# Kernel optimization log

Hardware: AMD Instinct MI355X
Metric: run time of the kernel (lower is better)

## Reference

```python
import jax, jax.numpy as jnp
import numpy as np

C = 256
CK = C // 8  # key/query channels


def setup_inputs() -> dict:
    key = jax.random.key(0)
    ks = jax.random.split(key, 7)
    B, H, W = 8, 64, 64
    x = jax.random.normal(ks[0], (B, C, H, W), dtype=jnp.float32)
    # 1x1 conv weights (out_ch, in_ch) and biases. Spectral norm is a weight
    # reparameterization; at forward time it is just a conv with (normalized)
    # weights, so we sample weights directly.
    Wf = jax.random.normal(ks[1], (CK, C), dtype=jnp.float32) * 0.02
    bf = jnp.zeros((CK,), dtype=jnp.float32)
    Wg = jax.random.normal(ks[2], (CK, C), dtype=jnp.float32) * 0.02
    bg = jnp.zeros((CK,), dtype=jnp.float32)
    Wh = jax.random.normal(ks[3], (C, C), dtype=jnp.float32) * 0.02
    bh = jnp.zeros((C,), dtype=jnp.float32)
    gamma = jnp.ones((1,), dtype=jnp.float32) * 0.5  # nonzero so attention path matters
    return {"x": x, "Wf": Wf, "bf": bf, "Wg": Wg, "bg": bg, "Wh": Wh, "bh": bh, "gamma": gamma}


def reference(x, Wf, bf, Wg, bg, Wh, bh, gamma):
    b, c, h, w = x.shape
    n = h * w
    xf = x.reshape(b, c, n)  # [B, C, N]
    # 1x1 convs == per-pixel linear maps
    fx = jnp.einsum("kc,bcn->bkn", Wf, xf) + bf[None, :, None]  # [B, CK, N]
    gx = jnp.einsum("kc,bcn->bkn", Wg, xf) + bg[None, :, None]  # [B, CK, N]
    hx = jnp.einsum("oc,bcn->bon", Wh, xf) + bh[None, :, None]  # [B, C, N]
    # sx[b, i, j] = <fx[:, i], gx[:, j]>
    sx = jnp.einsum("bki,bkj->bij", fx, gx)  # [B, N, N]
    # torch F.softmax(sx, dim=1): normalize over the first N axis (i)
    beta = jax.nn.softmax(sx, axis=1)
    ox = jnp.einsum("bci,bij->bcj", hx, beta).reshape(b, c, h, w)
    return gamma.reshape(()) * ox + x
```

## Files before the change

### kernel.cpp

```cpp
#include <hip/hip_runtime.h>
#include <stdint.h>


typedef __bf16 bf16;
typedef __bf16 bf16x2 __attribute__((ext_vector_type(2)));
typedef __bf16 bf16x8 __attribute__((ext_vector_type(8)));
typedef float  f32x16 __attribute__((ext_vector_type(16)));
typedef float  f32x4  __attribute__((ext_vector_type(4)));
typedef unsigned char u8;
typedef long   i64;

#define BATCH 8
#define CC    256
#define CKK   32
#define NN    4096
#define LOG2E 1.4426950408889634f

__device__ __forceinline__ f32x16 zero16() {
  f32x16 z;
#pragma unroll
  for (int i = 0; i < 16; ++i) z[i] = 0.0f;
  return z;
}

__device__ __forceinline__ unsigned pack2(float lo, float hi) {
  bf16x2 v = {(bf16)lo, (bf16)hi};
  return __builtin_bit_cast(unsigned, v);
}

__device__ __forceinline__ f32x16 mfma32(bf16x8 a, bf16x8 b, f32x16 c) {
  return __builtin_amdgcn_mfma_f32_32x32x16_bf16(a, b, c, 0, 0, 0);
}

__device__ __forceinline__ f32x16 mfma8(i64 a, i64 b, f32x16 c) {
  return __builtin_amdgcn_mfma_f32_32x32x16_fp8_fp8(a, b, c, 0, 0, 0);
}

#define GLDS16(srcp, dstp)                                                         \
  __builtin_amdgcn_global_load_lds(                                               \
      (const __attribute__((address_space(1))) void*)(srcp),                      \
      (__attribute__((address_space(3))) void*)(dstp), 16, 0, 0)

__global__ __launch_bounds__(256) void k_transpose(const float* __restrict__ x,
                                                   bf16* __restrict__ xT) {
  __shared__ float tile[64][65];
  const int n0 = blockIdx.x * 64;
  const int c0 = blockIdx.y * 64;
  const int b  = blockIdx.z;
  const int t = threadIdx.x;
  const int tn = t & 63, trow = t >> 6;
#pragma unroll
  for (int i = 0; i < 16; ++i) {
    int c = trow + i * 4;
    tile[c][tn] = x[((size_t)(b * CC + c0 + c)) * NN + n0 + tn];
  }
  __syncthreads();
#pragma unroll
  for (int i = 0; i < 16; ++i) {
    int n = trow + i * 4;
    xT[((size_t)(b * NN + n0 + n)) * CC + c0 + tn] = (bf16)tile[tn][n];
  }
}

__global__ __launch_bounds__(64) void k_wprep(const float* __restrict__ Wf, const float* __restrict__ bfv,
                                              const float* __restrict__ Wg, const float* __restrict__ bg,
                                              const float* __restrict__ Wh, const float* __restrict__ bh,
                                              bf16* __restrict__ Wcat, float* __restrict__ bcat) {
  const int ko = blockIdx.x;
  const int t = threadIdx.x;
  const float* src;
  float scale = 1.0f;
  if (ko < 32) src = Wf + (size_t)ko * CC;
  else if (ko < 64) { src = Wg + (size_t)(ko - 32) * CC; scale = LOG2E; }
  else src = Wh + (size_t)(ko - 64) * CC;
#pragma unroll
  for (int i = 0; i < 4; ++i)
    Wcat[(size_t)ko * CC + t + i * 64] = (bf16)(src[t + i * 64] * scale);
  if (ko == 0) {
    for (int i = t; i < 320; i += 64) {
      float v = (i < 32) ? bfv[i] : (i < 64) ? bg[i - 32] * LOG2E : bh[i - 64];
      bcat[i] = v;
    }
  }
}

__global__ __launch_bounds__(256, 2) void k_proj(const bf16* __restrict__ xT,
                                                 const bf16* __restrict__ Wcat,
                                                 const float* __restrict__ bcat,
                                                 bf16* __restrict__ fxT, bf16* __restrict__ gxT,
                                                 u8* __restrict__ hx8) {
  const int d = blockIdx.x;
  const int half = d >> 8;
  const int r = d & 255;
  const int b = r & 7, nb = r >> 3;
  const int t = threadIdx.x;
  const int w = t >> 6, ln = t & 63, ln31 = ln & 31, h = ln >> 5;
  const int n = nb * 128 + w * 32 + ln31;

  f32x16 acc[5];
#pragma unroll
  for (int m = 0; m < 5; ++m) acc[m] = zero16();

  const bf16* xrow = xT + ((size_t)(b * NN + n)) * CC;
#pragma unroll
  for (int ks = 0; ks < 16; ++ks) {
    bf16x8 bfrag = *(const bf16x8*)(xrow + ks * 16 + h * 8);
#pragma unroll
    for (int m = 0; m < 5; ++m) {
      const int mt = half * 5 + m;
      bf16x8 afrag = *(const bf16x8*)(Wcat + (size_t)(mt * 32 + ln31) * CC + ks * 16 + h * 8);
      acc[m] = mfma32(afrag, bfrag, acc[m]);
    }
  }

#pragma unroll
  for (int m = 0; m < 5; ++m) {
    const int mt = half * 5 + m;
#pragma unroll
    for (int q = 0; q < 4; ++q) {
      const int ko0 = mt * 32 + 8 * q + 4 * h;
      float v0 = acc[m][4 * q + 0] + bcat[ko0 + 0];
      float v1 = acc[m][4 * q + 1] + bcat[ko0 + 1];
      float v2 = acc[m][4 * q + 2] + bcat[ko0 + 2];
      float v3 = acc[m][4 * q + 3] + bcat[ko0 + 3];
      if (mt < 2) {
        bf16* dst = (mt == 0 ? fxT : gxT) + ((size_t)(b * NN + n)) * CKK + (8 * q + 4 * h);
        uint2 pv;
        pv.x = pack2(v0, v1);
        pv.y = pack2(v2, v3);
        *(uint2*)dst = pv;
      } else {
        const int c = ko0 - 64;
        unsigned wpk = (unsigned)__builtin_amdgcn_cvt_pk_fp8_f32(v0, v1, 0, false);
        wpk = (unsigned)__builtin_amdgcn_cvt_pk_fp8_f32(v2, v3, (int)wpk, true);
        u8* hp = hx8 + ((size_t)(b * CC + c)) * NN + n;
        hp[0]      = (u8)(wpk & 0xff);
        hp[NN]     = (u8)((wpk >> 8) & 0xff);
        hp[2 * NN] = (u8)((wpk >> 16) & 0xff);
        hp[3 * NN] = (u8)(wpk >> 24);
      }
    }
  }
}

__global__ __launch_bounds__(512, 2) void k_attn(const bf16* __restrict__ fxT,
                                                 const bf16* __restrict__ gxT,
                                                 const u8* __restrict__ hx8,
                                                 const float* __restrict__ x,
                                                 const float* __restrict__ gammap,
                                                 float* __restrict__ out) {
  extern __shared__ __align__(16) char smem[];
  __shared__ float lsh[128];
  const int d = blockIdx.x;
  const int b = d & 7, jb = d >> 3;
  const int t = threadIdx.x;
  const int g = t >> 8;
  const int tg = t & 255;
  const int wg = tg >> 6;
  const int ln = t & 63, ln31 = ln & 31, h = ln >> 5;
  const int j = jb * 128 + wg * 32 + ln31;
  const int kbase = g * 2048;

  const bf16* fxb = fxT + (size_t)b * NN * CKK;
  const u8*   hxb = hx8 + (size_t)b * CC * NN;

  u8*   vsg = (u8*)smem + g * 32768;
  bf16* ksg = (bf16*)(smem + 65536) + g * 8192;

  const bf16* qrow = gxT + ((size_t)b * NN + j) * CKK;
  bf16x8 qf0 = *(const bf16x8*)(qrow + h * 8);
  bf16x8 qf1 = *(const bf16x8*)(qrow + 16 + h * 8);
  asm volatile("" ::: "memory");

  int voff8[4];
#pragma unroll
  for (int ks = 0; ks < 4; ++ks)
    voff8[ks] = ln31 * 64 + (((ks + (ln31 >> 1)) & 3) * 16) + 8 * h;
  const int tk = (ln31 >> 1) & 3;
  const int ko0 = ln31 * 32 + ((h ^ tk) * 8);
  const int ko1 = ln31 * 32 + (((2 + h) ^ tk) * 8);

  const int vm = ((ln & 3) - (ln >> 3)) & 3;
  const u8* vlane8 = hxb + (size_t)(wg * 64 + (ln >> 2)) * NN + vm * 16;
  const int krow_l = ln >> 2;
  const int kcol_l = ((ln & 3) ^ ((ln >> 3) & 3)) * 8;
  const bf16* klane = fxb + (size_t)(wg * 16 + krow_l) * CKK + kcol_l;

#define STAGEV(slot, i0s)                                                     \
  {                                                                            \
    _Pragma("unroll")                                                          \
    for (int q = 0; q < 4; ++q)                                                \
      GLDS16(vlane8 + (size_t)q * 16 * NN + (i0s),                             \
             vsg + (slot) * 16384 + (wg * 4 + q) * 1024);                      \
  }
#define STAGEK(kslot, i0s)                                                    \
  { GLDS16(klane + (size_t)(i0s) * CKK, ksg + (kslot) * 2048 + wg * 512); }

  f32x16 oacc[8];
#pragma unroll
  for (int ct = 0; ct < 8; ++ct) oacc[ct] = zero16();
  const f32x16 vzero = zero16();
  float l_run = 0.0f;
  i64 pf[4] = {};

  auto QK = [&](int kslot, f32x16& s0, f32x16& s1) {
    const bf16* kt = ksg + kslot * 2048;
    bf16x8 kf00 = *(const bf16x8*)(kt + ko0);
    bf16x8 kf01 = *(const bf16x8*)(kt + ko1);
    bf16x8 kf10 = *(const bf16x8*)(kt + 1024 + ko0);
    bf16x8 kf11 = *(const bf16x8*)(kt + 1024 + ko1);
    s0 = mfma32(kf01, qf1, mfma32(kf00, qf0, vzero));
    s1 = mfma32(kf11, qf1, mfma32(kf10, qf0, vzero));
  };
  auto SM = [&](const f32x16& s0, const f32x16& s1) {
    float e0[16], e1[16];
#pragma unroll
    for (int r = 0; r < 16; ++r) e0[r] = __builtin_exp2f(s0[r]);
#pragma unroll
    for (int r = 0; r < 16; ++r) e1[r] = __builtin_exp2f(s1[r]);
    float ls0 = 0.0f, ls1 = 0.0f, ls2 = 0.0f, ls3 = 0.0f;
#pragma unroll
    for (int r = 0; r < 4; ++r) {
      ls0 += e0[r];      ls1 += e0[4 + r];
      ls2 += e0[8 + r];  ls3 += e0[12 + r];
      ls0 += e1[r];      ls1 += e1[4 + r];
      ls2 += e1[8 + r];  ls3 += e1[12 + r];
    }
    l_run += (ls0 + ls1) + (ls2 + ls3);
    unsigned pk4[8];
#pragma unroll
    for (int A = 0; A < 4; ++A) {
      unsigned w = (unsigned)__builtin_amdgcn_cvt_pk_fp8_f32(e0[4 * A], e0[4 * A + 1], 0, false);
      pk4[A] = (unsigned)__builtin_amdgcn_cvt_pk_fp8_f32(e0[4 * A + 2], e0[4 * A + 3], (int)w, true);
    }
#pragma unroll
    for (int A = 0; A < 4; ++A) {
      unsigned w = (unsigned)__builtin_amdgcn_cvt_pk_fp8_f32(e1[4 * A], e1[4 * A + 1], 0, false);
      pk4[4 + A] = (unsigned)__builtin_amdgcn_cvt_pk_fp8_f32(e1[4 * A + 2], e1[4 * A + 3], (int)w, true);
    }
#pragma unroll
    for (int f = 0; f < 4; ++f) {
      unsigned xw = pk4[2 * f], yw = pk4[2 * f + 1];
      asm("v_permlane32_swap_b32 %0, %1" : "+v"(xw), "+v"(yw));
      pf[f] = (i64)(((unsigned long long)yw << 32) | xw);
    }
  };
  auto PV = [&](int slot) {
    const u8* vb = vsg + slot * 16384;
    i64 va0, va1, va2, va3, vn0, vn1, vn2, vn3;
    va0 = *(const i64*)(vb + voff8[0]);
    va1 = *(const i64*)(vb + voff8[1]);
    va2 = *(const i64*)(vb + voff8[2]);
    va3 = *(const i64*)(vb + voff8[3]);
#pragma unroll
    for (int ct = 0; ct < 8; ++ct) {
      if (ct < 7) {
        const u8* vrow = vb + (ct + 1) * 2048;
        vn0 = *(const i64*)(vrow + voff8[0]);
        vn1 = *(const i64*)(vrow + voff8[1]);
        vn2 = *(const i64*)(vrow + voff8[2]);
        vn3 = *(const i64*)(vrow + voff8[3]);
      }
      oacc[ct] = mfma8(va0, pf[0], oacc[ct]);
      oacc[ct] = mfma8(va1, pf[1], oacc[ct]);
      oacc[ct] = mfma8(va2, pf[2], oacc[ct]);
      oacc[ct] = mfma8(va3, pf[3], oacc[ct]);
      va0 = vn0; va1 = vn1; va2 = vn2; va3 = vn3;
    }
  };

  STAGEK(0, kbase);
  STAGEV(0, kbase);
  STAGEK(1, kbase + 64);

  for (int kb = 0; kb < 32; ++kb) {
    asm volatile("s_waitcnt vmcnt(5)" ::: "memory");
    __builtin_amdgcn_s_barrier();
    asm volatile("" ::: "memory");

    f32x16 s0, s1;
    if (g == 0) {
      QK(kb & 3, s0, s1);
      SM(s0, s1);
    } else if (kb > 0) {
      PV((kb - 1) & 1);
    }

    asm volatile("s_waitcnt vmcnt(1)" ::: "memory");
    __builtin_amdgcn_s_barrier();
    asm volatile("" ::: "memory");

    STAGEV((kb + 1) & 1, kbase + ((kb + 1) & 31) * 64);
    STAGEK((kb + 2) & 3, kbase + ((kb + 2) & 31) * 64);

    if (g == 0) {
      PV(kb & 1);
    } else {
      QK(kb & 3, s0, s1);
      SM(s0, s1);
    }
  }
  if (g == 1) PV(31 & 1);

  l_run += __shfl_xor(l_run, 32);

  asm volatile("s_waitcnt vmcnt(0) lgkmcnt(0)" ::: "memory");
  __builtin_amdgcn_s_barrier();
  asm volatile("" ::: "memory");

  float* obuf = (float*)smem;
  const int jl = wg * 32 + ln31;
  if (g == 1) {
#pragma unroll
    for (int ct = 0; ct < 8; ++ct)
#pragma unroll
      for (int q = 0; q < 4; ++q) {
        f32x4 v;
        v[0] = oacc[ct][4 * q + 0];
        v[1] = oacc[ct][4 * q + 1];
        v[2] = oacc[ct][4 * q + 2];
        v[3] = oacc[ct][4 * q + 3];
        *(f32x4*)&obuf[jl * 260 + ct * 32 + 8 * q + 4 * h] = v;
      }
    if (h == 0) lsh[jl] = l_run;
  }
  __syncthreads();
  if (g == 0) {
    const float l = l_run + lsh[jl];
    const float ginv = gammap[0] / l;
    const float* xb = x + (size_t)b * CC * NN;
    float* ob = out + (size_t)b * CC * NN;
#pragma unroll
    for (int ct = 0; ct < 8; ++ct)
#pragma unroll
      for (int q = 0; q < 4; ++q) {
        f32x4 vB = *(const f32x4*)&obuf[jl * 260 + ct * 32 + 8 * q + 4 * h];
#pragma unroll
        for (int s = 0; s < 4; ++s) {
          int c = ct * 32 + 8 * q + 4 * h + s;
          size_t idx = (size_t)c * NN + j;
          float val = oacc[ct][4 * q + s] + vB[s];
          ob[idx] = fmaf(ginv, val, xb[idx]);
        }
      }
  }
#undef STAGEV
#undef STAGEK
}

extern "C" void kernel_launch(void* const* d_in, const int* in_sizes, int n_in,
                              void* d_out, int out_size, void* d_ws, size_t ws_size,
                              hipStream_t stream) {
  const float* x     = (const float*)d_in[0];
  const float* Wf    = (const float*)d_in[1];
  const float* bfv   = (const float*)d_in[2];
  const float* Wg    = (const float*)d_in[3];
  const float* bg    = (const float*)d_in[4];
  const float* Wh    = (const float*)d_in[5];
  const float* bh    = (const float*)d_in[6];
  const float* gamma = (const float*)d_in[7];
  float* out = (float*)d_out;

  char* ws = (char*)d_ws;
  bf16* fxT  = (bf16*)(ws);
  bf16* gxT  = (bf16*)(ws + 2097152);
  u8*   hx8  = (u8*)(ws + 4194304);
  bf16* Wcat = (bf16*)(ws + 12582912);
  float* bcat = (float*)(ws + 12746752);
  bf16* xT = (bf16*)d_out;

  k_transpose<<<dim3(64, 4, 8), 256, 0, stream>>>(x, xT);
  k_wprep<<<dim3(320), 64, 0, stream>>>(Wf, bfv, Wg, bg, Wh, bh, Wcat, bcat);
  k_proj<<<dim3(512), 256, 0, stream>>>(xT, Wcat, bcat, fxT, gxT, hx8);
  k_attn<<<dim3(256), 512, 133120, stream>>>(fxT, gxT, hx8, x, gamma, out);
}
```

Measured before the change: 120.9 us.

## Process two key tiles per barrier phase with deeper V/K staging

Restructures the attention main loop so each barrier phase handles two 64-key tiles instead of one, doubling the V shared-memory ring to four slots and keeping two P fragments in registers. This halves the number of barrier pairs and issues larger batches of global-to-LDS loads per phase, which is meant to cut synchronisation overhead and improve load/compute overlap between the two warp groups. In exchange, shared memory rises to 160KB per block and the row-sum buffer moves into dynamic LDS. The waitcnt placement is tightened to vmcnt(0), which may expose load latency, and the larger LDS footprint could lower occupancy or fail to launch if it exceeds the per-CU limit.

After: 140.4 us. 16.2% more time.

```diff
diff --git a/kernel.cpp b/kernel.cpp
--- a/kernel.cpp
+++ b/kernel.cpp
@@ -150,7 +150,6 @@
                                                  const float* __restrict__ gammap,
                                                  float* __restrict__ out) {
   extern __shared__ __align__(16) char smem[];
-  __shared__ float lsh[128];
   const int d = blockIdx.x;
   const int b = d & 7, jb = d >> 3;
   const int t = threadIdx.x;
@@ -164,8 +163,8 @@
   const bf16* fxb = fxT + (size_t)b * NN * CKK;
   const u8*   hxb = hx8 + (size_t)b * CC * NN;
 
-  u8*   vsg = (u8*)smem + g * 32768;
-  bf16* ksg = (bf16*)(smem + 65536) + g * 8192;
+  u8*   vsg = (u8*)smem + g * 65536;
+  bf16* ksg = (bf16*)(smem + 131072) + g * 8192;
 
   const bf16* qrow = gxT + ((size_t)b * NN + j) * CKK;
   bf16x8 qf0 = *(const bf16x8*)(qrow + h * 8);
@@ -201,7 +200,7 @@
   for (int ct = 0; ct < 8; ++ct) oacc[ct] = zero16();
   const f32x16 vzero = zero16();
   float l_run = 0.0f;
-  i64 pf[4] = {};
+  i64 pfA[4] = {}, pfB[4] = {};
 
   auto QK = [&](int kslot, f32x16& s0, f32x16& s1) {
     const bf16* kt = ksg + kslot * 2048;
@@ -212,7 +211,7 @@
     s0 = mfma32(kf01, qf1, mfma32(kf00, qf0, vzero));
     s1 = mfma32(kf11, qf1, mfma32(kf10, qf0, vzero));
   };
-  auto SM = [&](const f32x16& s0, const f32x16& s1) {
+  auto SM = [&](const f32x16& s0, const f32x16& s1, i64* pf) {
     float e0[16], e1[16];
 #pragma unroll
     for (int r = 0; r < 16; ++r) e0[r] = __builtin_exp2f(s0[r]);
@@ -245,7 +244,7 @@
       pf[f] = (i64)(((unsigned long long)yw << 32) | xw);
     }
   };
-  auto PV = [&](int slot) {
+  auto PV = [&](int slot, const i64* pf) {
     const u8* vb = vsg + slot * 16384;
     i64 va0, va1, va2, va3, vn0, vn1, vn2, vn3;
     va0 = *(const i64*)(vb + voff8[0]);
@@ -270,37 +269,49 @@
   };
 
   STAGEK(0, kbase);
+  STAGEK(1, kbase + 64);
   STAGEV(0, kbase);
-  STAGEK(1, kbase + 64);
-
-  for (int kb = 0; kb < 32; ++kb) {
-    asm volatile("s_waitcnt vmcnt(5)" ::: "memory");
+  STAGEV(1, kbase + 64);
+
+  for (int tt = 0; tt < 16; ++tt) {
+    const int k0 = 2 * tt;
+
+    asm volatile("s_waitcnt vmcnt(8)" ::: "memory");
     __builtin_amdgcn_s_barrier();
     asm volatile("" ::: "memory");
 
-    f32x16 s0, s1;
     if (g == 0) {
-      QK(kb & 3, s0, s1);
-      SM(s0, s1);
-    } else if (kb > 0) {
-      PV((kb - 1) & 1);
-    }
-
-    asm volatile("s_waitcnt vmcnt(1)" ::: "memory");
+      f32x16 s0, s1;
+      QK(k0 & 3, s0, s1);       SM(s0, s1, pfA);
+      QK((k0 + 1) & 3, s0, s1); SM(s0, s1, pfB);
+    } else if (tt > 0) {
+      PV((k0 - 2) & 3, pfA);
+      PV((k0 - 1) & 3, pfB);
+    }
+
+    asm volatile("s_waitcnt vmcnt(0)" ::: "memory");
     __builtin_amdgcn_s_barrier();
     asm volatile("" ::: "memory");
 
-    STAGEV((kb + 1) & 1, kbase + ((kb + 1) & 31) * 64);
-    STAGEK((kb + 2) & 3, kbase + ((kb + 2) & 31) * 64);
+    STAGEK((k0 + 2) & 3, kbase + ((k0 + 2) & 31) * 64);
+    STAGEK((k0 + 3) & 3, kbase + ((k0 + 3) & 31) * 64);
+    STAGEV((k0 + 2) & 3, kbase + ((k0 + 2) & 31) * 64);
+    STAGEV((k0 + 3) & 3, kbase + ((k0 + 3) & 31) * 64);
 
     if (g == 0) {
-      PV(kb & 1);
+      PV(k0 & 3, pfA);
+      PV((k0 + 1) & 3, pfB);
     } else {
-      QK(kb & 3, s0, s1);
-      SM(s0, s1);
-    }
-  }
-  if (g == 1) PV(31 & 1);
+      f32x16 s0, s1;
+      QK(k0 & 3, s0, s1);       SM(s0, s1, pfA);
+      QK((k0 + 1) & 3, s0, s1); SM(s0, s1, pfB);
+    }
+  }
+  if (g == 1) {
+    asm volatile("s_waitcnt vmcnt(0)" ::: "memory");
+    PV(2, pfA);
+    PV(3, pfB);
+  }
 
   l_run += __shfl_xor(l_run, 32);
 
@@ -309,6 +320,7 @@
   asm volatile("" ::: "memory");
 
   float* obuf = (float*)smem;
+  float* lsh  = (float*)(smem + 134400);
   const int jl = wg * 32 + ln31;
   if (g == 1) {
 #pragma unroll
@@ -372,5 +384,5 @@
   k_transpose<<<dim3(64, 4, 8), 256, 0, stream>>>(x, xT);
   k_wprep<<<dim3(320), 64, 0, stream>>>(Wf, bfv, Wg, bg, Wh, bh, Wcat, bcat);
   k_proj<<<dim3(512), 256, 0, stream>>>(xT, Wcat, bcat, fxT, gxT, hx8);
-  k_attn<<<dim3(256), 512, 133120, stream>>>(fxT, gxT, hx8, x, gamma, out);
-}
+  k_attn<<<dim3(256), 512, 163840, stream>>>(fxT, gxT, hx8, x, gamma, out);
+}
```
